# Performance work log

Hardware: AMD Instinct MI355X
Metric: run time of the kernel (lower is better)

## Reference

```python
import jax, jax.numpy as jnp
import numpy as np

B, C, H, W = 32, 1024, 28, 28
TEXT_DIM = 768
ATTN_DIM = 256
REDUCTION = 16
RED = max(1, C // REDUCTION)


def setup_inputs() -> dict:
    key = jax.random.key(0)
    ks = jax.random.split(key, 8)
    x = jax.random.normal(ks[0], (B, C, H, W), dtype=jnp.float32)
    text_feat = jax.random.normal(ks[1], (B, TEXT_DIM), dtype=jnp.float32)
    # ChannelAttention shared MLP (Linear weights, torch layout [out, in], no bias)
    w1 = jax.random.normal(ks[2], (RED, C), dtype=jnp.float32) * (1.0 / np.sqrt(C))
    w2 = jax.random.normal(ks[3], (C, RED), dtype=jnp.float32) * (1.0 / np.sqrt(RED))
    # TextGuidedSpatialAttention projections
    wq = jax.random.normal(ks[4], (ATTN_DIM, TEXT_DIM), dtype=jnp.float32) * 0.001
    wk = jax.random.normal(ks[5], (ATTN_DIM, C), dtype=jnp.float32) * np.sqrt(2.0 / ATTN_DIM)
    wv = jax.random.normal(ks[6], (ATTN_DIM, C), dtype=jnp.float32) * np.sqrt(2.0 / ATTN_DIM)
    wo = jax.random.normal(ks[7], (1, ATTN_DIM), dtype=jnp.float32) * np.sqrt(2.0)
    return {"x": x, "text_feat": text_feat, "w1": w1, "w2": w2,
            "wq": wq, "wk": wk, "wv": wv, "wo": wo}


def _forward(x, text_feat, w1, w2, wq, wk, wv, wo):
    b, c, h, w = x.shape
    # ----- Channel attention -----
    avg = jnp.mean(x, axis=(2, 3))          # [B, C]
    mx = jnp.max(x, axis=(2, 3))            # [B, C]
    def mlp(z):
        return jax.nn.relu(z @ w1.T) @ w2.T  # [B, C]
    ch_attn = jax.nn.sigmoid(mlp(avg) + mlp(mx))   # [B, C]
    x = x * ch_attn[:, :, None, None]
    # ----- Text-guided spatial attention -----
    q = text_feat @ wq.T                     # [B, A]
    # 1x1 conv == channel contraction
    k = jnp.einsum('ac,bchw->bahw', wk, x).reshape(b, ATTN_DIM, h * w)  # [B, A, N]
    v = jnp.einsum('ac,bchw->bahw', wv, x).reshape(b, ATTN_DIM, h * w)  # [B, A, N]
    scores = jnp.einsum('ba,ban->bn', q, k) / jnp.sqrt(jnp.float32(ATTN_DIM))  # [B, N]
    attn_weights = jax.nn.softmax(scores, axis=-1)                      # [B, N]
    attended = jnp.einsum('bn,ban->ba', attn_weights, v)                # [B, A]
    # out_proj 1x1 conv on a spatially-constant tensor == scalar per batch, broadcast
    spatial_scalar = jax.nn.sigmoid(attended @ wo.T)                    # [B, 1]
    spatial_attn = jnp.broadcast_to(spatial_scalar[:, :, None, None], (b, 1, h, w))
    return x * spatial_attn, spatial_attn


def reference(x, text_feat, w1, w2, wq, wk, wv, wo):
    return _forward(x, text_feat, w1, w2, wq, wk, wv, wo)
```

## Files before the change

### kernel.cpp

```cpp
#include <hip/hip_runtime.h>
#include <math.h>

#define B_   32
#define C_   1024
#define N_   784
#define NF4  196
#define TD   768
#define AD   256
#define RED_ 64
#define OUT0 25690112
#define ROWS (B_*C_)
#define SCH  64

#define OFF_AVG  0
#define OFF_MAX  32768
#define OFF_CA   65536
#define OFF_Q    98304
#define OFF_HS   106496
#define OFF_G    108544
#define OFF_WVO  141312
#define OFF_ATTN 142336
#define OFF_T    167424
#define OFF_S    200192
#define OFF_PART 200224

__global__ void k_avgmax(const float* __restrict__ x, float* __restrict__ avg,
                         float* __restrict__ mx) {
    int wave = threadIdx.x >> 6, lane = threadIdx.x & 63;
    int row0 = blockIdx.x * 8 + wave * 2;
    const float4* r0 = (const float4*)(x + (size_t)row0 * N_);
    const float4* r1 = r0 + NF4;
    float s0 = 0.f, s1 = 0.f, m0 = -3.4e38f, m1 = -3.4e38f;
    #pragma unroll
    for (int j = 0; j < 3; ++j) {
        int i = lane + 64 * j;
        float4 v0 = r0[i], v1 = r1[i];
        s0 += v0.x + v0.y + v0.z + v0.w;
        s1 += v1.x + v1.y + v1.z + v1.w;
        m0 = fmaxf(m0, fmaxf(fmaxf(v0.x, v0.y), fmaxf(v0.z, v0.w)));
        m1 = fmaxf(m1, fmaxf(fmaxf(v1.x, v1.y), fmaxf(v1.z, v1.w)));
    }
    if (lane < 4) {
        float4 v0 = r0[192 + lane], v1 = r1[192 + lane];
        s0 += v0.x + v0.y + v0.z + v0.w;
        s1 += v1.x + v1.y + v1.z + v1.w;
        m0 = fmaxf(m0, fmaxf(fmaxf(v0.x, v0.y), fmaxf(v0.z, v0.w)));
        m1 = fmaxf(m1, fmaxf(fmaxf(v1.x, v1.y), fmaxf(v1.z, v1.w)));
    }
    for (int o = 32; o; o >>= 1) {
        s0 += __shfl_down(s0, o, 64);
        s1 += __shfl_down(s1, o, 64);
        m0 = fmaxf(m0, __shfl_down(m0, o, 64));
        m1 = fmaxf(m1, __shfl_down(m1, o, 64));
    }
    if (lane == 0) {
        avg[row0]     = s0 * (1.f / (float)N_); mx[row0]     = m0;
        avg[row0 + 1] = s1 * (1.f / (float)N_); mx[row0 + 1] = m1;
    }
}

__global__ void k_proj(const float* __restrict__ text, const float* __restrict__ wq,
                       const float* __restrict__ avg, const float* __restrict__ mx,
                       const float* __restrict__ w1, const float* __restrict__ wv,
                       const float* __restrict__ wo, float* __restrict__ q,
                       float* __restrict__ hs, float* __restrict__ wvo) {
    int blk  = blockIdx.x;
    int wave = threadIdx.x >> 6, lane = threadIdx.x & 63;
    if (blk < 2048) {
        int w = blk * 4 + wave;
        int b = w >> 8, a = w & 255;
        const float4* tb = (const float4*)(text + (size_t)b * TD);
        const float4* wr = (const float4*)(wq + (size_t)a * TD);
        float acc = 0.f;
        #pragma unroll
        for (int j = 0; j < 3; ++j) {
            int i = lane + 64 * j;
            float4 tv = tb[i], wvv = wr[i];
            acc += tv.x * wvv.x + tv.y * wvv.y + tv.z * wvv.z + tv.w * wvv.w;
        }
        for (int o = 32; o; o >>= 1) acc += __shfl_down(acc, o, 64);
        if (lane == 0) q[(size_t)b * AD + a] = acc;
    } else if (blk < 2560) {
        int w = (blk - 2048) * 4 + wave;
        int b = w >> 6, r = w & 63;
        const float4* av = (const float4*)(avg + (size_t)b * C_);
        const float4* mv = (const float4*)(mx + (size_t)b * C_);
        const float4* wr = (const float4*)(w1 + (size_t)r * C_);
        float aa = 0.f, am = 0.f;
        #pragma unroll
        for (int j = 0; j < 4; ++j) {
            int i = lane + 64 * j;
            float4 wvv = wr[i], a4 = av[i], m4 = mv[i];
            aa += wvv.x * a4.x + wvv.y * a4.y + wvv.z * a4.z + wvv.w * a4.w;
            am += wvv.x * m4.x + wvv.y * m4.y + wvv.z * m4.z + wvv.w * m4.w;
        }
        for (int o = 32; o; o >>= 1) {
            aa += __shfl_down(aa, o, 64);
            am += __shfl_down(am, o, 64);
        }
        if (lane == 0) hs[(size_t)b * RED_ + r] = fmaxf(aa, 0.f) + fmaxf(am, 0.f);
    } else {
        int c = (blk - 2560) * 256 + threadIdx.x;
        float acc = 0.f;
        for (int a = 0; a < AD; ++a) acc += wo[a] * wv[(size_t)a * C_ + c];
        wvo[c] = acc;
    }
}

__global__ void k_cag(const float* __restrict__ hs, const float* __restrict__ w2,
                      const float* __restrict__ q, const float* __restrict__ wk,
                      float* __restrict__ ca, float* __restrict__ g) {
    int b = blockIdx.y;
    int t = threadIdx.x;
    int c = blockIdx.x * 256 + t;
    __shared__ float qs[AD];
    __shared__ float hss[RED_];
    qs[t] = q[(size_t)b * AD + t];
    if (t < RED_) hss[t] = hs[(size_t)b * RED_ + t];
    __syncthreads();
    float a1 = 0.f;
    #pragma unroll
    for (int r = 0; r < RED_; ++r) a1 += hss[r] * w2[(size_t)c * RED_ + r];
    float cav = 1.f / (1.f + __expf(-a1));
    ca[(size_t)b * C_ + c] = cav;
    float a2 = 0.f;
    #pragma unroll 8
    for (int a = 0; a < AD; ++a) a2 += qs[a] * wk[(size_t)a * C_ + c];
    g[(size_t)b * C_ + c] = a2 * cav * 0.0625f;
}

__global__ void k_scores(const float* __restrict__ x, const float* __restrict__ g,
                         float* __restrict__ part) {
    int chunk = blockIdx.x;
    int b     = blockIdx.y;
    int t     = threadIdx.x;
    int wave  = t >> 6, lane = t & 63;
    __shared__ float gs[16];
    __shared__ float4 l4[4 * NF4];
    if (t < 16) gs[t] = g[(size_t)b * C_ + chunk * 16 + t];
    __syncthreads();
    const float4* xb4 = (const float4*)(x +
        ((size_t)b * C_ + (size_t)chunk * 16 + (size_t)wave * 4) * N_);
    float4 a0 = {0,0,0,0}, a1 = {0,0,0,0}, a2 = {0,0,0,0}, a3 = {0,0,0,0};
    #pragma unroll
    for (int c = 0; c < 4; ++c) {
        float gv = gs[wave * 4 + c];
        const float4* row = xb4 + (size_t)c * NF4;
        float4 v;
        v = row[lane];       a0.x += gv*v.x; a0.y += gv*v.y; a0.z += gv*v.z; a0.w += gv*v.w;
        v = row[lane + 64];  a1.x += gv*v.x; a1.y += gv*v.y; a1.z += gv*v.z; a1.w += gv*v.w;
        v = row[lane + 128]; a2.x += gv*v.x; a2.y += gv*v.y; a2.z += gv*v.z; a2.w += gv*v.w;
        if (lane < 4) {
            v = row[lane + 192]; a3.x += gv*v.x; a3.y += gv*v.y; a3.z += gv*v.z; a3.w += gv*v.w;
        }
    }
    l4[wave * NF4 + lane]       = a0;
    l4[wave * NF4 + lane + 64]  = a1;
    l4[wave * NF4 + lane + 128] = a2;
    if (lane < 4) l4[wave * NF4 + lane + 192] = a3;
    __syncthreads();
    if (t < NF4) {
        float4 s0 = l4[t], s1 = l4[NF4 + t], s2 = l4[2 * NF4 + t], s3 = l4[3 * NF4 + t];
        float4 r;
        r.x = s0.x + s1.x + s2.x + s3.x;
        r.y = s0.y + s1.y + s2.y + s3.y;
        r.z = s0.z + s1.z + s2.z + s3.z;
        r.w = s0.w + s1.w + s2.w + s3.w;
        ((float4*)(part + ((size_t)b * SCH + chunk) * N_))[t] = r;
    }
}

__global__ void k_softmax(const float* __restrict__ part, float* __restrict__ attn) {
    int b = blockIdx.x;
    int t = threadIdx.x;
    int lane = t & 63, wave = t >> 6;
    const float* p = part + (size_t)b * SCH * N_;
    float v0 = 0.f, v1 = 0.f, v2 = 0.f, v3 = 0.f;
    for (int ch = 0; ch < SCH; ++ch) {
        const float* pc = p + (size_t)ch * N_;
        v0 += pc[t]; v1 += pc[t + 256]; v2 += pc[t + 512];
        if (t < 16) v3 += pc[t + 768];
    }
    float m = fmaxf(fmaxf(v0, v1), v2);
    if (t < 16) m = fmaxf(m, v3);
    for (int o = 32; o; o >>= 1) m = fmaxf(m, __shfl_down(m, o, 64));
    __shared__ float rm[4], rs[4];
    if (lane == 0) rm[wave] = m;
    __syncthreads();
    float M = fmaxf(fmaxf(rm[0], rm[1]), fmaxf(rm[2], rm[3]));
    float e0 = __expf(v0 - M), e1 = __expf(v1 - M), e2 = __expf(v2 - M);
    float e3 = (t < 16) ? __expf(v3 - M) : 0.f;
    float ssum = e0 + e1 + e2 + e3;
    for (int o = 32; o; o >>= 1) ssum += __shfl_down(ssum, o, 64);
    if (lane == 0) rs[wave] = ssum;
    __syncthreads();
    float inv = 1.f / (rs[0] + rs[1] + rs[2] + rs[3]);
    float* ab = attn + (size_t)b * N_;
    ab[t] = e0 * inv; ab[t + 256] = e1 * inv; ab[t + 512] = e2 * inv;
    if (t < 16) ab[t + 768] = e3 * inv;
}

__global__ void k_attend(const float* __restrict__ x, const float* __restrict__ attn,
                         const float* __restrict__ chattn, const float* __restrict__ wvo,
                         float* __restrict__ t_out) {
    int wave = threadIdx.x >> 6, lane = threadIdx.x & 63;
    int row0 = blockIdx.x * 8 + wave * 2;
    int b    = row0 >> 10;
    const float4* r0 = (const float4*)(x + (size_t)row0 * N_);
    const float4* r1 = r0 + NF4;
    const float4* ar = (const float4*)(attn + (size_t)b * N_);
    float s0 = 0.f, s1 = 0.f;
    #pragma unroll
    for (int j = 0; j < 3; ++j) {
        int i = lane + 64 * j;
        float4 av = ar[i];
        float4 v0 = r0[i], v1 = r1[i];
        s0 += v0.x * av.x + v0.y * av.y + v0.z * av.z + v0.w * av.w;
        s1 += v1.x * av.x + v1.y * av.y + v1.z * av.z + v1.w * av.w;
    }
    if (lane < 4) {
        float4 av = ar[192 + lane];
        float4 v0 = r0[192 + lane], v1 = r1[192 + lane];
        s0 += v0.x * av.x + v0.y * av.y + v0.z * av.z + v0.w * av.w;
        s1 += v1.x * av.x + v1.y * av.y + v1.z * av.z + v1.w * av.w;
    }
    for (int o = 32; o; o >>= 1) {
        s0 += __shfl_down(s0, o, 64);
        s1 += __shfl_down(s1, o, 64);
    }
    if (lane == 0) {
        int c0 = row0 & 1023;
        t_out[row0]     = s0 * chattn[row0]     * wvo[c0];
        t_out[row0 + 1] = s1 * chattn[row0 + 1] * wvo[c0 + 1];
    }
}

__global__ void k_scalar(const float* __restrict__ t_in, float* __restrict__ s_out) {
    int b    = blockIdx.x * 4 + (threadIdx.x >> 6);
    int lane = threadIdx.x & 63;
    const float4* tb = (const float4*)(t_in + (size_t)b * C_);
    float acc = 0.f;
    #pragma unroll
    for (int j = 0; j < 4; ++j) {
        float4 tv = tb[lane + 64 * j];
        acc += tv.x + tv.y + tv.z + tv.w;
    }
    for (int o = 32; o; o >>= 1) acc += __shfl_down(acc, o, 64);
    if (lane == 0) s_out[b] = 1.f / (1.f + __expf(-acc));
}

__global__ void k_finalize(const float* __restrict__ x, const float* __restrict__ chattn,
                           const float* __restrict__ s, float* __restrict__ out) {
    int blk = blockIdx.x;
    if (blk < ROWS / 8) {
        int wave = threadIdx.x >> 6, lane = threadIdx.x & 63;
        int row0 = blk * 8 + wave * 2;
        int b    = row0 >> 10;
        float sb  = s[b];
        float sc0 = chattn[row0] * sb;
        float sc1 = chattn[row0 + 1] * sb;
        const float4* r0 = (const float4*)(x + (size_t)row0 * N_);
        const float4* r1 = r0 + NF4;
        float4* o0 = (float4*)(out + (size_t)row0 * N_);
        float4* o1 = o0 + NF4;
        #pragma unroll
        for (int j = 0; j < 3; ++j) {
            int i = lane + 64 * j;
            float4 v0 = r0[i], v1 = r1[i];
            v0.x *= sc0; v0.y *= sc0; v0.z *= sc0; v0.w *= sc0;
            v1.x *= sc1; v1.y *= sc1; v1.z *= sc1; v1.w *= sc1;
            o0[i] = v0; o1[i] = v1;
        }
        if (lane < 4) {
            int i = 192 + lane;
            float4 v0 = r0[i], v1 = r1[i];
            v0.x *= sc0; v0.y *= sc0; v0.z *= sc0; v0.w *= sc0;
            v1.x *= sc1; v1.y *= sc1; v1.z *= sc1; v1.w *= sc1;
            o0[i] = v0; o1[i] = v1;
        }
    } else {
        int idx = (blk - ROWS / 8) * 256 + threadIdx.x;
        if (idx < (B_ * N_) / 4) {
            int b = idx / (N_ / 4);
            float v = s[b];
            ((float4*)(out + OUT0))[idx] = make_float4(v, v, v, v);
        }
    }
}

extern "C" void kernel_launch(void* const* d_in, const int* in_sizes, int n_in,
                              void* d_out, int out_size, void* d_ws, size_t ws_size,
                              hipStream_t stream) {
    const float* x    = (const float*)d_in[0];
    const float* text = (const float*)d_in[1];
    const float* w1   = (const float*)d_in[2];
    const float* w2   = (const float*)d_in[3];
    const float* wq   = (const float*)d_in[4];
    const float* wk   = (const float*)d_in[5];
    const float* wv   = (const float*)d_in[6];
    const float* wo   = (const float*)d_in[7];
    float* out = (float*)d_out;
    float* ws  = (float*)d_ws;

    float* avg  = ws + OFF_AVG;
    float* mx   = ws + OFF_MAX;
    float* ca   = ws + OFF_CA;
    float* q    = ws + OFF_Q;
    float* hs   = ws + OFF_HS;
    float* g    = ws + OFF_G;
    float* wvo  = ws + OFF_WVO;
    float* attn = ws + OFF_ATTN;
    float* tt   = ws + OFF_T;
    float* sv   = ws + OFF_S;
    float* part = ws + OFF_PART;

    k_avgmax<<<ROWS / 8, 256, 0, stream>>>(x, avg, mx);
    k_proj<<<2564, 256, 0, stream>>>(text, wq, avg, mx, w1, wv, wo, q, hs, wvo);
    k_cag<<<dim3(C_ / 256, B_), 256, 0, stream>>>(hs, w2, q, wk, ca, g);
    k_scores<<<dim3(SCH, B_), 256, 0, stream>>>(x, g, part);
    k_softmax<<<B_, 256, 0, stream>>>(part, attn);
    k_attend<<<ROWS / 8, 256, 0, stream>>>(x, attn, ca, wvo, tt);
    k_scalar<<<B_ / 4, 256, 0, stream>>>(tt, sv);
    k_finalize<<<ROWS / 8 + 25, 256, 0, stream>>>(x, ca, sv, out);
}
```

Baseline: 296.9 us.

## Fuse channel-gate, scores, softmax and attend into one pass over x

Merges the channel-gate/query projection, score computation, softmax, attended-value reduction and scalar sigmoid into one kernel. Scores and the per-pixel value projection (wvo times channel gate) come from a single read of x, and the last block per batch, found with an atomic counter, does the softmax-weighted reduction. This drops a full pass over x (the old attend kernel) and four launches. In exchange it adds a completion-counter protocol with threadfences, and 16 chunks per batch means only 512 blocks in the fused kernel.

```diff
diff --git a/kernel.cpp b/kernel.cpp
--- a/kernel.cpp
+++ b/kernel.cpp
@@ -10,19 +10,19 @@
 #define RED_ 64
 #define OUT0 25690112
 #define ROWS (B_*C_)
-#define SCH  64
+#define CH_  16
+#define CPB  64
 
 #define OFF_AVG  0
 #define OFF_MAX  32768
 #define OFF_CA   65536
 #define OFF_Q    98304
 #define OFF_HS   106496
-#define OFF_G    108544
-#define OFF_WVO  141312
-#define OFF_ATTN 142336
-#define OFF_T    167424
-#define OFF_S    200192
-#define OFF_PART 200224
+#define OFF_WVO  108544
+#define OFF_SV   109568
+#define OFF_CNT  109600
+#define OFF_PS   109632
+#define OFF_PY   511040
 
 __global__ void k_avgmax(const float* __restrict__ x, float* __restrict__ avg,
                          float* __restrict__ mx) {
@@ -63,9 +63,11 @@
                        const float* __restrict__ avg, const float* __restrict__ mx,
                        const float* __restrict__ w1, const float* __restrict__ wv,
                        const float* __restrict__ wo, float* __restrict__ q,
-                       float* __restrict__ hs, float* __restrict__ wvo) {
+                       float* __restrict__ hs, float* __restrict__ wvo,
+                       int* __restrict__ cnt) {
     int blk  = blockIdx.x;
     int wave = threadIdx.x >> 6, lane = threadIdx.x & 63;
+    __shared__ float red[256];
     if (blk < 2048) {
         int w = blk * 4 + wave;
         int b = w >> 8, a = w & 255;
@@ -99,154 +101,153 @@
             am += __shfl_down(am, o, 64);
         }
         if (lane == 0) hs[(size_t)b * RED_ + r] = fmaxf(aa, 0.f) + fmaxf(am, 0.f);
+    } else if (blk < 2576) {
+        int local = blk - 2560;
+        int t = threadIdx.x;
+        int cl = t & 63, sl = t >> 6;
+        int c = local * 64 + cl;
+        const float* wvp = wv + (size_t)(sl * 64) * C_ + c;
+        float acc = 0.f;
+        #pragma unroll 8
+        for (int a = 0; a < 64; ++a) acc += wo[sl * 64 + a] * wvp[(size_t)a * C_];
+        red[t] = acc;
+        __syncthreads();
+        if (t < 64) wvo[local * 64 + t] = red[t] + red[64 + t] + red[128 + t] + red[192 + t];
     } else {
-        int c = (blk - 2560) * 256 + threadIdx.x;
-        float acc = 0.f;
-        for (int a = 0; a < AD; ++a) acc += wo[a] * wv[(size_t)a * C_ + c];
-        wvo[c] = acc;
-    }
-}
-
-__global__ void k_cag(const float* __restrict__ hs, const float* __restrict__ w2,
-                      const float* __restrict__ q, const float* __restrict__ wk,
-                      float* __restrict__ ca, float* __restrict__ g) {
-    int b = blockIdx.y;
-    int t = threadIdx.x;
-    int c = blockIdx.x * 256 + t;
+        if (threadIdx.x < B_) cnt[threadIdx.x] = 0;
+    }
+}
+
+__global__ __launch_bounds__(256) void k_scores(
+        const float* __restrict__ x, const float* __restrict__ q,
+        const float* __restrict__ hs, const float* __restrict__ w2,
+        const float* __restrict__ wk, const float* __restrict__ wvo,
+        float* __restrict__ ca, float* __restrict__ partS, float* __restrict__ partY,
+        int* __restrict__ cnt, float* __restrict__ sv) {
+    int chunk = blockIdx.x, b = blockIdx.y, t = threadIdx.x;
+    int wave = t >> 6, lane = t & 63;
     __shared__ float qs[AD];
     __shared__ float hss[RED_];
+    __shared__ float redA[256], redB[256];
+    __shared__ float gsg[CPB], gsh[CPB];
+    __shared__ float4 l4s[4 * NF4], l4y[4 * NF4];
+    __shared__ float rm[4], rs[4], rd[4];
+    __shared__ int winflag;
+
     qs[t] = q[(size_t)b * AD + t];
     if (t < RED_) hss[t] = hs[(size_t)b * RED_ + t];
     __syncthreads();
-    float a1 = 0.f;
-    #pragma unroll
-    for (int r = 0; r < RED_; ++r) a1 += hss[r] * w2[(size_t)c * RED_ + r];
-    float cav = 1.f / (1.f + __expf(-a1));
-    ca[(size_t)b * C_ + c] = cav;
-    float a2 = 0.f;
-    #pragma unroll 8
-    for (int a = 0; a < AD; ++a) a2 += qs[a] * wk[(size_t)a * C_ + c];
-    g[(size_t)b * C_ + c] = a2 * cav * 0.0625f;
-}
-
-__global__ void k_scores(const float* __restrict__ x, const float* __restrict__ g,
-                         float* __restrict__ part) {
-    int chunk = blockIdx.x;
-    int b     = blockIdx.y;
-    int t     = threadIdx.x;
-    int wave  = t >> 6, lane = t & 63;
-    __shared__ float gs[16];
-    __shared__ float4 l4[4 * NF4];
-    if (t < 16) gs[t] = g[(size_t)b * C_ + chunk * 16 + t];
+    {
+        int cl = t & 63, sl = t >> 6;
+        int c  = chunk * CPB + cl;
+        const float* wkp = wk + (size_t)(sl * 64) * C_ + c;
+        float a2 = 0.f;
+        #pragma unroll 8
+        for (int a = 0; a < 64; ++a) a2 += qs[sl * 64 + a] * wkp[(size_t)a * C_];
+        redA[t] = a2;
+        const float* w2p = w2 + (size_t)c * RED_ + sl * 16;
+        float a1 = 0.f;
+        #pragma unroll
+        for (int r = 0; r < 16; ++r) a1 += hss[sl * 16 + r] * w2p[r];
+        redB[t] = a1;
+    }
+    __syncthreads();
+    if (t < CPB) {
+        float s2 = redA[t] + redA[64 + t] + redA[128 + t] + redA[192 + t];
+        float s1 = redB[t] + redB[64 + t] + redB[128 + t] + redB[192 + t];
+        float cav = 1.f / (1.f + __expf(-s1));
+        ca[(size_t)b * C_ + chunk * CPB + t] = cav;
+        gsg[t] = s2 * cav * 0.0625f;
+        gsh[t] = wvo[chunk * CPB + t] * cav;
+    }
     __syncthreads();
     const float4* xb4 = (const float4*)(x +
-        ((size_t)b * C_ + (size_t)chunk * 16 + (size_t)wave * 4) * N_);
-    float4 a0 = {0,0,0,0}, a1 = {0,0,0,0}, a2 = {0,0,0,0}, a3 = {0,0,0,0};
-    #pragma unroll
-    for (int c = 0; c < 4; ++c) {
-        float gv = gs[wave * 4 + c];
-        const float4* row = xb4 + (size_t)c * NF4;
+        ((size_t)b * C_ + (size_t)chunk * CPB + (size_t)wave * 16) * N_);
+    float4 z = make_float4(0.f, 0.f, 0.f, 0.f);
+    float4 s0 = z, s1v = z, s2v = z, s3 = z;
+    float4 y0 = z, y1 = z, y2 = z, y3 = z;
+    #pragma unroll 4
+    for (int cc = 0; cc < 16; ++cc) {
+        float gv = gsg[wave * 16 + cc], hv = gsh[wave * 16 + cc];
+        const float4* row = xb4 + (size_t)cc * NF4;
         float4 v;
-        v = row[lane];       a0.x += gv*v.x; a0.y += gv*v.y; a0.z += gv*v.z; a0.w += gv*v.w;
-        v = row[lane + 64];  a1.x += gv*v.x; a1.y += gv*v.y; a1.z += gv*v.z; a1.w += gv*v.w;
-        v = row[lane + 128]; a2.x += gv*v.x; a2.y += gv*v.y; a2.z += gv*v.z; a2.w += gv*v.w;
+        v = row[lane];
+        s0.x += gv*v.x; s0.y += gv*v.y; s0.z += gv*v.z; s0.w += gv*v.w;
+        y0.x += hv*v.x; y0.y += hv*v.y; y0.z += hv*v.z; y0.w += hv*v.w;
+        v = row[lane + 64];
+        s1v.x += gv*v.x; s1v.y += gv*v.y; s1v.z += gv*v.z; s1v.w += gv*v.w;
+        y1.x  += hv*v.x; y1.y  += hv*v.y; y1.z  += hv*v.z; y1.w  += hv*v.w;
+        v = row[lane + 128];
+        s2v.x += gv*v.x; s2v.y += gv*v.y; s2v.z += gv*v.z; s2v.w += gv*v.w;
+        y2.x  += hv*v.x; y2.y  += hv*v.y; y2.z  += hv*v.z; y2.w  += hv*v.w;
         if (lane < 4) {
-            v = row[lane + 192]; a3.x += gv*v.x; a3.y += gv*v.y; a3.z += gv*v.z; a3.w += gv*v.w;
-        }
-    }
-    l4[wave * NF4 + lane]       = a0;
-    l4[wave * NF4 + lane + 64]  = a1;
-    l4[wave * NF4 + lane + 128] = a2;
-    if (lane < 4) l4[wave * NF4 + lane + 192] = a3;
+            v = row[lane + 192];
+            s3.x += gv*v.x; s3.y += gv*v.y; s3.z += gv*v.z; s3.w += gv*v.w;
+            y3.x += hv*v.x; y3.y += hv*v.y; y3.z += hv*v.z; y3.w += hv*v.w;
+        }
+    }
+    l4s[wave * NF4 + lane]       = s0;
+    l4s[wave * NF4 + lane + 64]  = s1v;
+    l4s[wave * NF4 + lane + 128] = s2v;
+    l4y[wave * NF4 + lane]       = y0;
+    l4y[wave * NF4 + lane + 64]  = y1;
+    l4y[wave * NF4 + lane + 128] = y2;
+    if (lane < 4) {
+        l4s[wave * NF4 + lane + 192] = s3;
+        l4y[wave * NF4 + lane + 192] = y3;
+    }
     __syncthreads();
     if (t < NF4) {
-        float4 s0 = l4[t], s1 = l4[NF4 + t], s2 = l4[2 * NF4 + t], s3 = l4[3 * NF4 + t];
+        float4 a = l4s[t], bb = l4s[NF4 + t], c4 = l4s[2 * NF4 + t], d = l4s[3 * NF4 + t];
         float4 r;
-        r.x = s0.x + s1.x + s2.x + s3.x;
-        r.y = s0.y + s1.y + s2.y + s3.y;
-        r.z = s0.z + s1.z + s2.z + s3.z;
-        r.w = s0.w + s1.w + s2.w + s3.w;
-        ((float4*)(part + ((size_t)b * SCH + chunk) * N_))[t] = r;
-    }
-}
-
-__global__ void k_softmax(const float* __restrict__ part, float* __restrict__ attn) {
-    int b = blockIdx.x;
-    int t = threadIdx.x;
-    int lane = t & 63, wave = t >> 6;
-    const float* p = part + (size_t)b * SCH * N_;
+        r.x = a.x + bb.x + c4.x + d.x; r.y = a.y + bb.y + c4.y + d.y;
+        r.z = a.z + bb.z + c4.z + d.z; r.w = a.w + bb.w + c4.w + d.w;
+        ((float4*)(partS + ((size_t)b * CH_ + chunk) * N_))[t] = r;
+        a = l4y[t]; bb = l4y[NF4 + t]; c4 = l4y[2 * NF4 + t]; d = l4y[3 * NF4 + t];
+        r.x = a.x + bb.x + c4.x + d.x; r.y = a.y + bb.y + c4.y + d.y;
+        r.z = a.z + bb.z + c4.z + d.z; r.w = a.w + bb.w + c4.w + d.w;
+        ((float4*)(partY + ((size_t)b * CH_ + chunk) * N_))[t] = r;
+    }
+    __syncthreads();
+    if (t == 0) {
+        __threadfence();
+        winflag = (atomicAdd(&cnt[b], 1) == CH_ - 1) ? 1 : 0;
+    }
+    __syncthreads();
+    if (!winflag) return;
+    __threadfence();
+    const float* pS = partS + (size_t)b * CH_ * N_;
+    const float* pY = partY + (size_t)b * CH_ * N_;
     float v0 = 0.f, v1 = 0.f, v2 = 0.f, v3 = 0.f;
-    for (int ch = 0; ch < SCH; ++ch) {
-        const float* pc = p + (size_t)ch * N_;
-        v0 += pc[t]; v1 += pc[t + 256]; v2 += pc[t + 512];
-        if (t < 16) v3 += pc[t + 768];
+    float w0 = 0.f, w1v = 0.f, w2v = 0.f, w3 = 0.f;
+    for (int ch = 0; ch < CH_; ++ch) {
+        const float* pcs = pS + (size_t)ch * N_;
+        const float* pcy = pY + (size_t)ch * N_;
+        v0 += pcs[t]; v1 += pcs[t + 256]; v2 += pcs[t + 512];
+        w0 += pcy[t]; w1v += pcy[t + 256]; w2v += pcy[t + 512];
+        if (t < 16) { v3 += pcs[t + 768]; w3 += pcy[t + 768]; }
     }
     float m = fmaxf(fmaxf(v0, v1), v2);
     if (t < 16) m = fmaxf(m, v3);
     for (int o = 32; o; o >>= 1) m = fmaxf(m, __shfl_down(m, o, 64));
-    __shared__ float rm[4], rs[4];
     if (lane == 0) rm[wave] = m;
     __syncthreads();
     float M = fmaxf(fmaxf(rm[0], rm[1]), fmaxf(rm[2], rm[3]));
     float e0 = __expf(v0 - M), e1 = __expf(v1 - M), e2 = __expf(v2 - M);
     float e3 = (t < 16) ? __expf(v3 - M) : 0.f;
     float ssum = e0 + e1 + e2 + e3;
-    for (int o = 32; o; o >>= 1) ssum += __shfl_down(ssum, o, 64);
-    if (lane == 0) rs[wave] = ssum;
-    __syncthreads();
-    float inv = 1.f / (rs[0] + rs[1] + rs[2] + rs[3]);
-    float* ab = attn + (size_t)b * N_;
-    ab[t] = e0 * inv; ab[t + 256] = e1 * inv; ab[t + 512] = e2 * inv;
-    if (t < 16) ab[t + 768] = e3 * inv;
-}
-
-__global__ void k_attend(const float* __restrict__ x, const float* __restrict__ attn,
-                         const float* __restrict__ chattn, const float* __restrict__ wvo,
-                         float* __restrict__ t_out) {
-    int wave = threadIdx.x >> 6, lane = threadIdx.x & 63;
-    int row0 = blockIdx.x * 8 + wave * 2;
-    int b    = row0 >> 10;
-    const float4* r0 = (const float4*)(x + (size_t)row0 * N_);
-    const float4* r1 = r0 + NF4;
-    const float4* ar = (const float4*)(attn + (size_t)b * N_);
-    float s0 = 0.f, s1 = 0.f;
-    #pragma unroll
-    for (int j = 0; j < 3; ++j) {
-        int i = lane + 64 * j;
-        float4 av = ar[i];
-        float4 v0 = r0[i], v1 = r1[i];
-        s0 += v0.x * av.x + v0.y * av.y + v0.z * av.z + v0.w * av.w;
-        s1 += v1.x * av.x + v1.y * av.y + v1.z * av.z + v1.w * av.w;
-    }
-    if (lane < 4) {
-        float4 av = ar[192 + lane];
-        float4 v0 = r0[192 + lane], v1 = r1[192 + lane];
-        s0 += v0.x * av.x + v0.y * av.y + v0.z * av.z + v0.w * av.w;
-        s1 += v1.x * av.x + v1.y * av.y + v1.z * av.z + v1.w * av.w;
-    }
+    float dot  = e0 * w0 + e1 * w1v + e2 * w2v + e3 * w3;
     for (int o = 32; o; o >>= 1) {
-        s0 += __shfl_down(s0, o, 64);
-        s1 += __shfl_down(s1, o, 64);
-    }
-    if (lane == 0) {
-        int c0 = row0 & 1023;
-        t_out[row0]     = s0 * chattn[row0]     * wvo[c0];
-        t_out[row0 + 1] = s1 * chattn[row0 + 1] * wvo[c0 + 1];
-    }
-}
-
-__global__ void k_scalar(const float* __restrict__ t_in, float* __restrict__ s_out) {
-    int b    = blockIdx.x * 4 + (threadIdx.x >> 6);
-    int lane = threadIdx.x & 63;
-    const float4* tb = (const float4*)(t_in + (size_t)b * C_);
-    float acc = 0.f;
-    #pragma unroll
-    for (int j = 0; j < 4; ++j) {
-        float4 tv = tb[lane + 64 * j];
-        acc += tv.x + tv.y + tv.z + tv.w;
-    }
-    for (int o = 32; o; o >>= 1) acc += __shfl_down(acc, o, 64);
-    if (lane == 0) s_out[b] = 1.f / (1.f + __expf(-acc));
+        ssum += __shfl_down(ssum, o, 64);
+        dot  += __shfl_down(dot,  o, 64);
+    }
+    if (lane == 0) { rs[wave] = ssum; rd[wave] = dot; }
+    __syncthreads();
+    if (t == 0) {
+        float S = rs[0] + rs[1] + rs[2] + rs[3];
+        float D = rd[0] + rd[1] + rd[2] + rd[3];
+        sv[b] = 1.f / (1.f + __expf(-D / S));
+    }
 }
 
 __global__ void k_finalize(const float* __restrict__ x, const float* __restrict__ chattn,
@@ -302,24 +303,19 @@
     float* out = (float*)d_out;
     float* ws  = (float*)d_ws;
 
-    float* avg  = ws + OFF_AVG;
-    float* mx   = ws + OFF_MAX;
-    float* ca   = ws + OFF_CA;
-    float* q    = ws + OFF_Q;
-    float* hs   = ws + OFF_HS;
-    float* g    = ws + OFF_G;
-    float* wvo  = ws + OFF_WVO;
-    float* attn = ws + OFF_ATTN;
-    float* tt   = ws + OFF_T;
-    float* sv   = ws + OFF_S;
-    float* part = ws + OFF_PART;
+    float* avg   = ws + OFF_AVG;
+    float* mx    = ws + OFF_MAX;
+    float* ca    = ws + OFF_CA;
+    float* q     = ws + OFF_Q;
+    float* hs    = ws + OFF_HS;
+    float* wvo   = ws + OFF_WVO;
+    float* sv    = ws + OFF_SV;
+    int*   cnt   = (int*)(ws + OFF_CNT);
+    float* partS = ws + OFF_PS;
+    float* partY = ws + OFF_PY;
 
     k_avgmax<<<ROWS / 8, 256, 0, stream>>>(x, avg, mx);
-    k_proj<<<2564, 256, 0, stream>>>(text, wq, avg, mx, w1, wv, wo, q, hs, wvo);
-    k_cag<<<dim3(C_ / 256, B_), 256, 0, stream>>>(hs, w2, q, wk, ca, g);
-    k_scores<<<dim3(SCH, B_), 256, 0, stream>>>(x, g, part);
-    k_softmax<<<B_, 256, 0, stream>>>(part, attn);
-    k_attend<<<ROWS / 8, 256, 0, stream>>>(x, attn, ca, wvo, tt);
-    k_scalar<<<B_ / 4, 256, 0, stream>>>(tt, sv);
+    k_proj<<<2577, 256, 0, stream>>>(text, wq, avg, mx, w1, wv, wo, q, hs, wvo, cnt);
+    k_scores<<<dim3(CH_, B_), 256, 0, stream>>>(x, q, hs, w2, wk, wvo, ca, partS, partY, cnt, sv);
     k_finalize<<<ROWS / 8 + 25, 256, 0, stream>>>(x, ca, sv, out);
 }
```

Result: faster. 266.7 us (-10.2%).
